# Performance work log

Hardware: AMD Instinct MI355X
Metric: run time of the kernel (lower is better)

Reference implementation:

```python
import jax, jax.numpy as jnp
import numpy as np

# Qwen3-Next gated delta-net dims
H_K, H_V, DK, DV = 16, 32, 128, 128
HID, KCONV = 2048, 4
KEY_DIM, VALUE_DIM = H_K * DK, H_V * DV      # 2048, 4096
CONV_DIM = 2 * KEY_DIM + VALUE_DIM           # 8192
GV = H_V // H_K                              # v-heads per k-head = 2
EPS = 1e-6
SEQ = 4096


def setup_inputs() -> dict:
    key = jax.random.key(0)
    ks = jax.random.split(key, 8)
    n = lambda k, sh, s: jax.random.normal(k, sh, jnp.float32) * s
    return {
        "hidden_states": n(ks[0], (SEQ, HID), 1.0),
        "W_qkvz": n(ks[1], (HID, 2 * KEY_DIM + 2 * VALUE_DIM), HID ** -0.5),
        "W_ba": n(ks[2], (HID, 2 * H_V), HID ** -0.5),
        "conv_w": n(ks[3], (CONV_DIM, KCONV), 0.5),
        "A_log": jnp.log(jax.random.uniform(ks[4], (H_V,), jnp.float32, 1.0, 16.0)),
        "dt_bias": jnp.ones((H_V,), jnp.float32),
        "norm_weight": jnp.ones((DV,), jnp.float32),
        "W_out": n(ks[5], (VALUE_DIM, HID), VALUE_DIM ** -0.5),
    }


def _l2norm(x):
    return x * jax.lax.rsqrt(jnp.sum(x * x, -1, keepdims=True) + EPS)


def reference(hidden_states, W_qkvz, W_ba, conv_w, A_log, dt_bias, norm_weight, W_out):
    L = hidden_states.shape[0]
    # 1. input projections
    qkvz = hidden_states @ W_qkvz            # (L, 12288)
    ba = hidden_states @ W_ba                # (L, 64)
    # fix_query_key_value_ordering: view per k-head group then split
    qkvz = qkvz.reshape(L, H_K, 2 * DK + 2 * GV * DV)
    q = qkvz[:, :, :DK]                                         # (L, Hk, dk)
    k = qkvz[:, :, DK:2 * DK]                                   # (L, Hk, dk)
    v = qkvz[:, :, 2 * DK:2 * DK + GV * DV].reshape(L, H_V, DV)  # (L, Hv, dv)
    z = qkvz[:, :, 2 * DK + GV * DV:].reshape(L, H_V, DV)
    ba = ba.reshape(L, H_K, 2 * GV)
    b = ba[:, :, :GV].reshape(L, H_V)
    a = ba[:, :, GV:].reshape(L, H_V)

    # 2. causal depthwise conv1d over [q|k|v] channels + silu
    mixed = jnp.concatenate([q.reshape(L, KEY_DIM), k.reshape(L, KEY_DIM),
                             v.reshape(L, VALUE_DIM)], axis=-1)  # (L, CONV_DIM)
    xp = jnp.pad(mixed, ((KCONV - 1, 0), (0, 0)))
    conv = sum(xp[i:i + L] * conv_w[:, i] for i in range(KCONV))
    mixed = jax.nn.silu(conv)

    q = mixed[:, :KEY_DIM].reshape(L, H_K, DK)
    k = mixed[:, KEY_DIM:2 * KEY_DIM].reshape(L, H_K, DK)
    v = mixed[:, 2 * KEY_DIM:].reshape(L, H_V, DV)

    # 3. fused gating: g = -exp(A_log) * softplus(a + dt_bias); beta = sigmoid(b)
    g = -jnp.exp(A_log) * jax.nn.softplus(a + dt_bias)   # (L, Hv)
    beta = jax.nn.sigmoid(b)                              # (L, Hv)

    # qk l2-norm + scale, expand k-heads to v-heads (GQA repeat)
    q = jnp.repeat(_l2norm(q), GV, axis=1) * (DK ** -0.5)  # (L, Hv, dk)
    k = jnp.repeat(_l2norm(k), GV, axis=1)

    # 4. gated delta-rule recurrence over time (state per head: dk x dv)
    def step(S, inp):
        qt, kt, vt, gt, bt = inp
        S = S * jnp.exp(gt)[:, None, None]
        kv = jnp.einsum('hkv,hk->hv', S, kt)
        delta = (vt - kv) * bt[:, None]
        S = S + kt[:, :, None] * delta[:, None, :]
        return S, jnp.einsum('hkv,hk->hv', S, qt)

    S0 = jnp.zeros((H_V, DK, DV), jnp.float32)
    _, core = jax.lax.scan(step, S0, (q, k, v, g, beta))   # (L, Hv, dv)

    # 5. gated RMSNorm (norm before gate): rmsnorm(x)*w * silu(z)
    var = jnp.mean(core * core, -1, keepdims=True)
    core = core * jax.lax.rsqrt(var + EPS) * norm_weight
    core = core * jax.nn.silu(z)

    # 6. output projection
    return core.reshape(L, VALUE_DIM) @ W_out
```

## Files before the change

kernel.cpp:

```cpp
#include <hip/hip_runtime.h>
#include <hip/hip_bf16.h>

#define SEQ 4096
#define HID 2048
#define HK_ 16
#define HV_ 32
#define KEY_DIM 2048
#define VALUE_DIM 4096
#define CONV_DIM 8192
#define NQKVZ 12288

typedef unsigned short ushort_t;
typedef short bf16x8 __attribute__((ext_vector_type(8)));
typedef float f32x4 __attribute__((ext_vector_type(4)));
typedef float f32x2 __attribute__((ext_vector_type(2)));

__device__ __forceinline__ float bf2f(ushort_t h) {
    union { unsigned int u; float f; } x; x.u = ((unsigned int)h) << 16; return x.f;
}
__device__ __forceinline__ void cvt8(uint4 v, float* f) {
    unsigned int w[4] = {v.x, v.y, v.z, v.w};
#pragma unroll
    for (int i = 0; i < 4; i++) {
        union { unsigned int u; float f; } lo, hi;
        lo.u = w[i] << 16; hi.u = w[i] & 0xffff0000u;
        f[2 * i] = lo.f; f[2 * i + 1] = hi.f;
    }
}
__device__ __forceinline__ void cvt8v(uint4 v, f32x2* f) {
    unsigned int w[4] = {v.x, v.y, v.z, v.w};
#pragma unroll
    for (int i = 0; i < 4; i++) {
        union { unsigned int u; float f; } lo, hi;
        lo.u = w[i] << 16; hi.u = w[i] & 0xffff0000u;
        f[i] = (f32x2){lo.f, hi.f};
    }
}
__device__ __forceinline__ ushort_t f2bf(float f) {
    union { float f; unsigned int u; } x; x.f = f;
    unsigned int u = x.u;
    u += 0x7fffu + ((u >> 16) & 1u);
    return (ushort_t)(u >> 16);
}

__device__ __forceinline__ void gload_lds16(const void* g, void* l) {
    __builtin_amdgcn_global_load_lds(
        (const __attribute__((address_space(1))) void*)g,
        (__attribute__((address_space(3))) void*)l, 16, 0, 0);
}
__device__ __forceinline__ void gload_lds4(const void* g, void* l) {
    __builtin_amdgcn_global_load_lds(
        (const __attribute__((address_space(1))) void*)g,
        (__attribute__((address_space(3))) void*)l, 4, 0, 0);
}

template <int CTRL>
__device__ __forceinline__ float dpp_add(float x) {
    union { float f; int i; } a, b;
    a.f = x;
    b.i = __builtin_amdgcn_update_dpp(0, a.i, CTRL, 0xF, 0xF, true);
    return a.f + b.f;
}
__device__ __forceinline__ float red16(float x) {
    x = dpp_add<0xB1>(x);
    x = dpp_add<0x4E>(x);
    x = dpp_add<0x141>(x);
    x = dpp_add<0x140>(x);
    return x;
}

__global__ void k_cvt(const float* __restrict__ src, ushort_t* __restrict__ dst)
{
    size_t i = ((size_t)blockIdx.x * 256 + threadIdx.x) * 8;
    float4 a = *(const float4*)&src[i];
    float4 b = *(const float4*)&src[i + 4];
    ushort_t u[8];
    u[0]=f2bf(a.x); u[1]=f2bf(a.y); u[2]=f2bf(a.z); u[3]=f2bf(a.w);
    u[4]=f2bf(b.x); u[5]=f2bf(b.y); u[6]=f2bf(b.z); u[7]=f2bf(b.w);
    *(uint4*)&dst[i] = *(uint4*)u;
}

__global__ __launch_bounds__(256) void k_transpose(const float* __restrict__ src,
                                                   ushort_t* __restrict__ dst,
                                                   int R, int C)
{
    __shared__ float tile[64][65];
    int c0 = blockIdx.x * 64, r0 = blockIdx.y * 64;
    int t = threadIdx.x;
    int tr = t >> 4, tc = (t & 15) * 4;
#pragma unroll
    for (int r = 0; r < 4; r++) {
        float4 v = *(const float4*)&src[(size_t)(r0 + tr + r * 16) * C + c0 + tc];
        tile[tr + r * 16][tc + 0] = v.x;
        tile[tr + r * 16][tc + 1] = v.y;
        tile[tr + r * 16][tc + 2] = v.z;
        tile[tr + r * 16][tc + 3] = v.w;
    }
    __syncthreads();
#pragma unroll
    for (int r = 0; r < 4; r++) {
        int n = c0 + tr + r * 16;
        ushort_t u[4];
#pragma unroll
        for (int i = 0; i < 4; i++) u[i] = f2bf(tile[tc + i][tr + r * 16]);
        *(uint2*)&dst[(size_t)n * R + r0 + tc] = *(uint2*)u;
    }
}

__global__ void k_ba(const float* __restrict__ A, const float* __restrict__ B,
                     const float* __restrict__ A_log, const float* __restrict__ dt_bias,
                     float* __restrict__ gbf)
{
    __shared__ float As[16][132];
    __shared__ float Bs[16][68];
    int tid = threadIdx.x;
    int m0 = blockIdx.x * 128;
    int tx = tid & 15, ty = tid >> 4;
    int arow = tid >> 2, akq = tid & 3;
    int brow = tid >> 4, bc4 = tid & 15;
    float acc[8][4];
#pragma unroll
    for (int i = 0; i < 8; i++)
#pragma unroll
        for (int j = 0; j < 4; j++) acc[i][j] = 0.f;

    for (int k0 = 0; k0 < HID; k0 += 16) {
        float4 a0 = *(const float4*)&A[(size_t)(m0 + arow) * HID + k0 + akq * 4];
        float4 a1 = *(const float4*)&A[(size_t)(m0 + arow + 64) * HID + k0 + akq * 4];
        float4 b0 = *(const float4*)&B[(size_t)(k0 + brow) * 64 + bc4 * 4];
        __syncthreads();
        As[akq * 4 + 0][arow] = a0.x; As[akq * 4 + 1][arow] = a0.y;
        As[akq * 4 + 2][arow] = a0.z; As[akq * 4 + 3][arow] = a0.w;
        As[akq * 4 + 0][arow + 64] = a1.x; As[akq * 4 + 1][arow + 64] = a1.y;
        As[akq * 4 + 2][arow + 64] = a1.z; As[akq * 4 + 3][arow + 64] = a1.w;
        *(float4*)&Bs[brow][bc4 * 4] = b0;
        __syncthreads();
#pragma unroll
        for (int kk = 0; kk < 16; kk++) {
            float xa[8], yb[4];
            *(float4*)&xa[0] = *(const float4*)&As[kk][ty * 8];
            *(float4*)&xa[4] = *(const float4*)&As[kk][ty * 8 + 4];
            *(float4*)&yb[0] = *(const float4*)&Bs[kk][tx * 4];
#pragma unroll
            for (int i = 0; i < 8; i++)
#pragma unroll
                for (int j = 0; j < 4; j++) acc[i][j] += xa[i] * yb[j];
        }
    }
#pragma unroll
    for (int i = 0; i < 8; i++) {
        int t = m0 + ty * 8 + i;
#pragma unroll
        for (int j = 0; j < 4; j++) {
            int c = tx * 4 + j;
            int hk = c >> 2, rr = c & 3;
            float val = acc[i][j];
            if (rr < 2) {
                int hv = hk * 2 + rr;
                gbf[(t * HV_ + hv) * 2 + 1] = 1.f / (1.f + expf(-val));
            } else {
                int hv = hk * 2 + (rr - 2);
                float v2 = val + dt_bias[hv];
                float sp = (v2 > 20.f) ? v2 : log1pf(expf(v2));
                float g = -expf(A_log[hv]) * sp;
                gbf[(t * HV_ + hv) * 2 + 0] = expf(g);
            }
        }
    }
}

__global__ __launch_bounds__(256) void k_gemm_qkvz(const ushort_t* __restrict__ Ab,
                                                   const ushort_t* __restrict__ Bt,
                                                   ushort_t* __restrict__ preact,
                                                   ushort_t* __restrict__ zb)
{
    __shared__ ushort_t As[128][32];
    __shared__ ushort_t Bs[128][32];
    int tid = threadIdx.x;
    int m0 = blockIdx.y * 128, n0 = blockIdx.x * 128;
    int lane = tid & 63, wave = tid >> 6;
    int wm = (wave >> 1) * 64, wn = (wave & 1) * 64;
    int quad = lane >> 4, l16 = lane & 15;

    int srow = ((wave & 1) << 6) + (lane >> 2);
    int scol = (lane & 3) << 3;
    const ushort_t* gsrc = (wave < 2)
        ? &Ab[(size_t)(m0 + srow) * HID + scol]
        : &Bt[(size_t)(n0 + srow) * HID + scol];
    ushort_t* lbase = ((wave < 2) ? &As[0][0] : &Bs[0][0]) + ((wave & 1) << 11);

    f32x4 acc[4][4];
#pragma unroll
    for (int i = 0; i < 4; i++)
#pragma unroll
        for (int j = 0; j < 4; j++) acc[i][j] = (f32x4){0.f, 0.f, 0.f, 0.f};

    for (int k0 = 0; k0 < HID; k0 += 32) {
#pragma unroll
        for (int i = 0; i < 4; i++)
            gload_lds16(gsrc + k0 + (size_t)i * 16 * HID, lbase + i * 512);
        __syncthreads();
        bf16x8 af[4], bfr[4];
#pragma unroll
        for (int i = 0; i < 4; i++) af[i]  = *(bf16x8*)&As[wm + i * 16 + l16][quad * 8];
#pragma unroll
        for (int j = 0; j < 4; j++) bfr[j] = *(bf16x8*)&Bs[wn + j * 16 + l16][quad * 8];
#pragma unroll
        for (int i = 0; i < 4; i++)
#pragma unroll
            for (int j = 0; j < 4; j++)
                acc[i][j] = __builtin_amdgcn_mfma_f32_16x16x32_bf16(af[i], bfr[j], acc[i][j], 0, 0, 0);
        __syncthreads();
    }
    int hk = n0 / 768, r = n0 % 768;
    ushort_t* dst; int ldd;
    if (r < 128)      { dst = preact + hk * 128;                    ldd = CONV_DIM; }
    else if (r < 256) { dst = preact + 2048 + hk * 128;             ldd = CONV_DIM; }
    else if (r < 512) { dst = preact + 4096 + hk * 256 + (r - 256); ldd = CONV_DIM; }
    else              { dst = zb + hk * 256 + (r - 512);            ldd = VALUE_DIM; }
#pragma unroll
    for (int i = 0; i < 4; i++)
#pragma unroll
        for (int j = 0; j < 4; j++)
#pragma unroll
            for (int rg = 0; rg < 4; rg++) {
                int m = m0 + wm + i * 16 + quad * 4 + rg;
                int n = wn + j * 16 + l16;
                dst[(size_t)m * ldd + n] = f2bf(acc[i][j][rg]);
            }
}

__global__ __launch_bounds__(256) void k_gemm_out(const ushort_t* __restrict__ Ab,
                                                  const ushort_t* __restrict__ Bt,
                                                  float* __restrict__ C)
{
    __shared__ ushort_t As[128][32];
    __shared__ ushort_t Bs[128][32];
    int tid = threadIdx.x;
    int m0 = blockIdx.y * 128, n0 = blockIdx.x * 128;
    int lane = tid & 63, wave = tid >> 6;
    int wm = (wave >> 1) * 64, wn = (wave & 1) * 64;
    int quad = lane >> 4, l16 = lane & 15;

    int srow = ((wave & 1) << 6) + (lane >> 2);
    int scol = (lane & 3) << 3;
    const ushort_t* gsrc = (wave < 2)
        ? &Ab[(size_t)(m0 + srow) * VALUE_DIM + scol]
        : &Bt[(size_t)(n0 + srow) * VALUE_DIM + scol];
    ushort_t* lbase = ((wave < 2) ? &As[0][0] : &Bs[0][0]) + ((wave & 1) << 11);

    f32x4 acc[4][4];
#pragma unroll
    for (int i = 0; i < 4; i++)
#pragma unroll
        for (int j = 0; j < 4; j++) acc[i][j] = (f32x4){0.f, 0.f, 0.f, 0.f};

    for (int k0 = 0; k0 < VALUE_DIM; k0 += 32) {
#pragma unroll
        for (int i = 0; i < 4; i++)
            gload_lds16(gsrc + k0 + (size_t)i * 16 * VALUE_DIM, lbase + i * 512);
        __syncthreads();
        bf16x8 af[4], bfr[4];
#pragma unroll
        for (int i = 0; i < 4; i++) af[i]  = *(bf16x8*)&As[wm + i * 16 + l16][quad * 8];
#pragma unroll
        for (int j = 0; j < 4; j++) bfr[j] = *(bf16x8*)&Bs[wn + j * 16 + l16][quad * 8];
#pragma unroll
        for (int i = 0; i < 4; i++)
#pragma unroll
            for (int j = 0; j < 4; j++)
                acc[i][j] = __builtin_amdgcn_mfma_f32_16x16x32_bf16(af[i], bfr[j], acc[i][j], 0, 0, 0);
        __syncthreads();
    }
#pragma unroll
    for (int i = 0; i < 4; i++)
#pragma unroll
        for (int j = 0; j < 4; j++)
#pragma unroll
            for (int rg = 0; rg < 4; rg++) {
                int m = m0 + wm + i * 16 + quad * 4 + rg;
                int n = n0 + wn + j * 16 + l16;
                C[(size_t)m * HID + n] = acc[i][j][rg];
            }
}

__global__ __launch_bounds__(256) void k_conv(const ushort_t* __restrict__ pre,
                                              const float* __restrict__ cw,
                                              ushort_t* __restrict__ qn,
                                              ushort_t* __restrict__ kn,
                                              ushort_t* __restrict__ vv)
{
    int tid = threadIdx.x;
    int c = blockIdx.x * 2048 + tid * 8;
    int t0 = blockIdx.y * 4;
    float w[8][4];
#pragma unroll
    for (int j = 0; j < 8; j++)
        *(float4*)w[j] = *(const float4*)&cw[(size_t)(c + j) * 4];
    float p[7][8];
#pragma unroll
    for (int i = 0; i < 7; i++) {
        int tt = t0 + i - 3;
        if (tt >= 0) {
            uint4 v = *(const uint4*)&pre[(size_t)tt * CONV_DIM + c];
            cvt8(v, p[i]);
        } else {
#pragma unroll
            for (int j = 0; j < 8; j++) p[i][j] = 0.f;
        }
    }
    float x[4][8];
#pragma unroll
    for (int u = 0; u < 4; u++)
#pragma unroll
        for (int j = 0; j < 8; j++) {
            float a = p[u][j] * w[j][0] + p[u + 1][j] * w[j][1]
                    + p[u + 2][j] * w[j][2] + p[u + 3][j] * w[j][3];
            x[u][j] = a / (1.f + expf(-a));
        }
    if (blockIdx.x < 2) {
        bool isq = (blockIdx.x == 0);
        float headscale = isq ? 0.08838834764831845f : 1.f;
        ushort_t* dst = isq ? qn : kn;
        int cc = isq ? c : (c - KEY_DIM);
#pragma unroll
        for (int u = 0; u < 4; u++) {
            float ss = 0.f;
#pragma unroll
            for (int j = 0; j < 8; j++) ss += x[u][j] * x[u][j];
            ss = red16(ss);
            float mul = headscale / sqrtf(ss + 1e-6f);
            ushort_t o[8];
#pragma unroll
            for (int j = 0; j < 8; j++) o[j] = f2bf(x[u][j] * mul);
            *(uint4*)&dst[(size_t)(t0 + u) * KEY_DIM + cc] = *(uint4*)o;
        }
    } else {
        int cc = c - 2 * KEY_DIM;
#pragma unroll
        for (int u = 0; u < 4; u++) {
            ushort_t o[8];
#pragma unroll
            for (int j = 0; j < 8; j++) o[j] = f2bf(x[u][j]);
            *(uint4*)&vv[(size_t)(t0 + u) * VALUE_DIM + cc] = *(uint4*)o;
        }
    }
}

__global__ __launch_bounds__(256) void k_recur(const ushort_t* __restrict__ qn,
                                               const ushort_t* __restrict__ kn,
                                               const ushort_t* __restrict__ vv,
                                               const float2* __restrict__ gb,
                                               float* __restrict__ core)
{
    __shared__ ushort_t Ks[2][32][128];
    __shared__ ushort_t Qs[2][32][128];
    __shared__ ushort_t Vs[2][32][16];
    __shared__ float    Gs[2][32][2];
    int tid = threadIdx.x;
    int h = blockIdx.y;
    int hk = h >> 1;
    int kc = tid & 15;
    int cl = tid >> 4;
    bool lead = (kc == 0);
    int lane = tid & 63, wave = tid >> 6;

    const ushort_t* kh = kn + hk * 128;
    const ushort_t* qh = qn + hk * 128;
    const ushort_t* vh = vv + h * 128 + blockIdx.x * 16;
    const float*    gh = (const float*)(gb + h);
    float* outp = core + h * 128 + blockIdx.x * 16 + cl;

    auto stage = [&](int bi, int t0) {
        if (wave < 2) {
            int rb = wave * 16;
#pragma unroll
            for (int c = 0; c < 4; c++) {
                int r = rb + c * 4 + (lane >> 4);
                gload_lds16(kh + (size_t)(t0 + r) * KEY_DIM + (lane & 15) * 8,
                            &Ks[bi][rb + c * 4][0]);
            }
#pragma unroll
            for (int c = 0; c < 2; c++) {
                int r = rb + c * 8 + (lane >> 3);
                gload_lds4(vh + (size_t)(t0 + r) * VALUE_DIM + (lane & 7) * 2,
                           &Vs[bi][rb + c * 8][0]);
            }
        } else {
            int rb = (wave - 2) * 16;
#pragma unroll
            for (int c = 0; c < 4; c++) {
                int r = rb + c * 4 + (lane >> 4);
                gload_lds16(qh + (size_t)(t0 + r) * KEY_DIM + (lane & 15) * 8,
                            &Qs[bi][rb + c * 4][0]);
            }
            if (wave == 2) {
                int r = lane >> 1;
                gload_lds4(gh + (size_t)(t0 + r) * (HV_ * 2) + (lane & 1),
                           &Gs[bi][0][0]);
            }
        }
    };

    f32x2 S_[4];
#pragma unroll
    for (int j = 0; j < 4; j++) S_[j] = (f32x2){0.f, 0.f};

    stage(0, 0);
    __syncthreads();

    for (int tc = 0; tc < SEQ / 32; tc++) {
        int bi = tc & 1;
        if (tc + 1 < SEQ / 32) stage(bi ^ 1, (tc + 1) * 32);
        int t0 = tc * 32;
#pragma unroll 8
        for (int s = 0; s < 32; s++) {
            uint4 kvr = *(const uint4*)&Ks[bi][s][kc * 8];
            uint4 qvr = *(const uint4*)&Qs[bi][s][kc * 8];
            f32x2 k2[4], q2[4];
            cvt8v(kvr, k2);
            cvt8v(qvr, q2);
            float v_ = bf2f(Vs[bi][s][cl]);
            float e = Gs[bi][s][0], b = Gs[bi][s][1];
            f32x2 acc = S_[0] * k2[0];
            acc += S_[1] * k2[1];
            acc += S_[2] * k2[2];
            acc += S_[3] * k2[3];
            float d1 = red16(acc.x + acc.y);
            float dl = (v_ - e * d1) * b;
            f32x2 e2 = (f32x2){e, e}, dl2 = (f32x2){dl, dl};
            f32x2 oacc = (f32x2){0.f, 0.f};
#pragma unroll
            for (int j = 0; j < 4; j++) {
                S_[j] = S_[j] * e2 + k2[j] * dl2;
                oacc += S_[j] * q2[j];
            }
            float o = red16(oacc.x + oacc.y);
            if (lead) outp[(size_t)(t0 + s) * VALUE_DIM] = o;
        }
        __syncthreads();
    }
}

__global__ void k_gate(const float* __restrict__ core, const ushort_t* __restrict__ z,
                       const float* __restrict__ nw, ushort_t* __restrict__ corebf)
{
    __shared__ float red[2];
    int hv = blockIdx.x, t = blockIdx.y, d = threadIdx.x;
    size_t idx = (size_t)t * VALUE_DIM + hv * 128 + d;
    float cval = core[idx];
    float ss = cval * cval;
    for (int m = 32; m >= 1; m >>= 1) ss += __shfl_xor(ss, m, 64);
    int wv = d >> 6, ln = d & 63;
    if (ln == 0) red[wv] = ss;
    __syncthreads();
    float var = (red[0] + red[1]) * (1.f / 128.f);
    float zv = bf2f(z[idx]);
    float out = cval * (1.f / sqrtf(var + 1e-6f)) * nw[d] * (zv / (1.f + expf(-zv)));
    corebf[idx] = f2bf(out);
}

extern "C" void kernel_launch(void* const* d_in, const int* in_sizes, int n_in,
                              void* d_out, int out_size, void* d_ws, size_t ws_size,
                              hipStream_t stream)
{
    const float* hs    = (const float*)d_in[0];
    const float* Wqkvz = (const float*)d_in[1];
    const float* Wba   = (const float*)d_in[2];
    const float* convw = (const float*)d_in[3];
    const float* Alog  = (const float*)d_in[4];
    const float* dtb   = (const float*)d_in[5];
    const float* nw    = (const float*)d_in[6];
    const float* Wout  = (const float*)d_in[7];
    float* out = (float*)d_out;

    char* w = (char*)d_ws;
    ushort_t* preact = (ushort_t*)w;
    float*    coreb  = (float*)w;
    w += (size_t)SEQ * CONV_DIM * 2;
    ushort_t* zb = (ushort_t*)w;  w += (size_t)SEQ * VALUE_DIM * 2;
    float* gbf   = (float*)w;     w += (size_t)SEQ * HV_ * 8;
    ushort_t* qnb = (ushort_t*)w; w += (size_t)SEQ * KEY_DIM * 2;
    ushort_t* knb = (ushort_t*)w; w += (size_t)SEQ * KEY_DIM * 2;
    ushort_t* vvb = (ushort_t*)w; w += (size_t)SEQ * VALUE_DIM * 2;
    size_t needed = (size_t)(w - (char*)d_ws);
    if (ws_size < needed) return;

    ushort_t* wqT    = qnb;
    ushort_t* hsb    = qnb + (size_t)24 * 1024 * 1024;
    ushort_t* woutT  = vvb;
    ushort_t* corebf = qnb;

    hipLaunchKernelGGL(k_ba, dim3(32), dim3(256), 0, stream, hs, Wba, Alog, dtb, gbf);
    hipLaunchKernelGGL(k_cvt, dim3(4096), dim3(256), 0, stream, hs, hsb);
    hipLaunchKernelGGL(k_transpose, dim3(192, 32), dim3(256), 0, stream, Wqkvz, wqT, HID, NQKVZ);
    hipLaunchKernelGGL(k_gemm_qkvz, dim3(96, 32), dim3(256), 0, stream, hsb, wqT, preact, zb);
    hipLaunchKernelGGL(k_conv, dim3(4, 1024), dim3(256), 0, stream, preact, convw, qnb, knb, vvb);
    hipLaunchKernelGGL(k_recur, dim3(8, 32), dim3(256), 0, stream, qnb, knb, vvb,
                       (const float2*)gbf, coreb);
    hipLaunchKernelGGL(k_transpose, dim3(32, 64), dim3(256), 0, stream, Wout, woutT, VALUE_DIM, HID);
    hipLaunchKernelGGL(k_gate, dim3(32, 4096), dim3(128), 0, stream, coreb, zb, nw, corebf);
    hipLaunchKernelGGL(k_gemm_out, dim3(16, 32), dim3(256), 0, stream, corebf, woutT, out);
}
```

Before: 1.561 ms.

## Process both GQA v-heads per block in recurrence to share K/Q loads

The recurrence kernel now handles the two value heads that share one key head inside a single block: each thread keeps two state slices and reuses the same K and Q vectors from shared memory for both. Blocks shrink to 128 threads covering 8 value columns per head, on a 16x16 grid, so the total block count stays at 256. This halves redundant K/Q global and LDS traffic per unit of work and adds independent instruction streams per thread to hide reduction latency. The cost is fewer threads per block, more registers, and longer serial per-step work per thread.

```diff
diff --git a/kernel.cpp b/kernel.cpp
--- a/kernel.cpp
+++ b/kernel.cpp
@@ -347,7 +347,7 @@
     }
 }
 
-__global__ __launch_bounds__(256) void k_recur(const ushort_t* __restrict__ qn,
+__global__ __launch_bounds__(128) void k_recur(const ushort_t* __restrict__ qn,
                                                const ushort_t* __restrict__ kn,
                                                const ushort_t* __restrict__ vv,
                                                const float2* __restrict__ gb,
@@ -355,56 +355,57 @@
 {
     __shared__ ushort_t Ks[2][32][128];
     __shared__ ushort_t Qs[2][32][128];
-    __shared__ ushort_t Vs[2][32][16];
-    __shared__ float    Gs[2][32][2];
+    __shared__ ushort_t Vs[2][32][2][8];
+    __shared__ float    Gs[2][32][2][2];
     int tid = threadIdx.x;
-    int h = blockIdx.y;
-    int hk = h >> 1;
+    int hp = blockIdx.y;
     int kc = tid & 15;
     int cl = tid >> 4;
     bool lead = (kc == 0);
     int lane = tid & 63, wave = tid >> 6;
 
-    const ushort_t* kh = kn + hk * 128;
-    const ushort_t* qh = qn + hk * 128;
-    const ushort_t* vh = vv + h * 128 + blockIdx.x * 16;
-    const float*    gh = (const float*)(gb + h);
-    float* outp = core + h * 128 + blockIdx.x * 16 + cl;
+    const ushort_t* kh = kn + hp * 128;
+    const ushort_t* qh = qn + hp * 128;
+    const ushort_t* vh = vv + (size_t)(2 * hp) * 128 + blockIdx.x * 8;
+    const float*    gh = (const float*)gb;
+    float* outp0 = core + (size_t)(2 * hp) * 128 + blockIdx.x * 8 + cl;
+    float* outp1 = outp0 + 128;
 
     auto stage = [&](int bi, int t0) {
-        if (wave < 2) {
-            int rb = wave * 16;
+        if (wave == 0) {
+#pragma unroll
+            for (int c = 0; c < 8; c++) {
+                int r = c * 4 + (lane >> 4);
+                gload_lds16(kh + (size_t)(t0 + r) * KEY_DIM + (lane & 15) * 8,
+                            &Ks[bi][c * 4][0]);
+            }
 #pragma unroll
             for (int c = 0; c < 4; c++) {
-                int r = rb + c * 4 + (lane >> 4);
-                gload_lds16(kh + (size_t)(t0 + r) * KEY_DIM + (lane & 15) * 8,
-                            &Ks[bi][rb + c * 4][0]);
+                int u = c * 64 + lane;
+                int t = u >> 3, hh = (u >> 2) & 1, cp = u & 3;
+                gload_lds4(vh + (size_t)(t0 + t) * VALUE_DIM + hh * 128 + cp * 2,
+                           &Vs[bi][c * 8][0][0]);
+            }
+        } else {
+#pragma unroll
+            for (int c = 0; c < 8; c++) {
+                int r = c * 4 + (lane >> 4);
+                gload_lds16(qh + (size_t)(t0 + r) * KEY_DIM + (lane & 15) * 8,
+                            &Qs[bi][c * 4][0]);
             }
 #pragma unroll
             for (int c = 0; c < 2; c++) {
-                int r = rb + c * 8 + (lane >> 3);
-                gload_lds4(vh + (size_t)(t0 + r) * VALUE_DIM + (lane & 7) * 2,
-                           &Vs[bi][rb + c * 8][0]);
-            }
-        } else {
-            int rb = (wave - 2) * 16;
-#pragma unroll
-            for (int c = 0; c < 4; c++) {
-                int r = rb + c * 4 + (lane >> 4);
-                gload_lds16(qh + (size_t)(t0 + r) * KEY_DIM + (lane & 15) * 8,
-                            &Qs[bi][rb + c * 4][0]);
-            }
-            if (wave == 2) {
-                int r = lane >> 1;
-                gload_lds4(gh + (size_t)(t0 + r) * (HV_ * 2) + (lane & 1),
-                           &Gs[bi][0][0]);
+                int u = c * 64 + lane;
+                int t = u >> 2, hh = (u >> 1) & 1, ww = u & 1;
+                gload_lds4(gh + ((size_t)(t0 + t) * HV_ + 2 * hp + hh) * 2 + ww,
+                           &Gs[bi][c * 16][0][0]);
             }
         }
     };
 
-    f32x2 S_[4];
-#pragma unroll
-    for (int j = 0; j < 4; j++) S_[j] = (f32x2){0.f, 0.f};
+    f32x2 S0_[4], S1_[4];
+#pragma unroll
+    for (int j = 0; j < 4; j++) { S0_[j] = (f32x2){0.f, 0.f}; S1_[j] = (f32x2){0.f, 0.f}; }
 
     stage(0, 0);
     __syncthreads();
@@ -420,23 +421,37 @@
             f32x2 k2[4], q2[4];
             cvt8v(kvr, k2);
             cvt8v(qvr, q2);
-            float v_ = bf2f(Vs[bi][s][cl]);
-            float e = Gs[bi][s][0], b = Gs[bi][s][1];
-            f32x2 acc = S_[0] * k2[0];
-            acc += S_[1] * k2[1];
-            acc += S_[2] * k2[2];
-            acc += S_[3] * k2[3];
-            float d1 = red16(acc.x + acc.y);
-            float dl = (v_ - e * d1) * b;
-            f32x2 e2 = (f32x2){e, e}, dl2 = (f32x2){dl, dl};
-            f32x2 oacc = (f32x2){0.f, 0.f};
+            float v0 = bf2f(Vs[bi][s][0][cl]);
+            float v1 = bf2f(Vs[bi][s][1][cl]);
+            float e0 = Gs[bi][s][0][0], b0 = Gs[bi][s][0][1];
+            float e1 = Gs[bi][s][1][0], b1 = Gs[bi][s][1][1];
+            f32x2 aA0 = S0_[0] * k2[0];
+            f32x2 aA1 = S1_[0] * k2[0];
+#pragma unroll
+            for (int j = 1; j < 4; j++) {
+                aA0 += S0_[j] * k2[j];
+                aA1 += S1_[j] * k2[j];
+            }
+            float rA0 = red16(aA0.x + aA0.y);
+            float rA1 = red16(aA1.x + aA1.y);
+            float dl0 = (v0 - e0 * rA0) * b0;
+            float dl1 = (v1 - e1 * rA1) * b1;
+            f32x2 e20 = (f32x2){e0, e0}, dl20 = (f32x2){dl0, dl0};
+            f32x2 e21 = (f32x2){e1, e1}, dl21 = (f32x2){dl1, dl1};
+            f32x2 oa0 = (f32x2){0.f, 0.f}, oa1 = (f32x2){0.f, 0.f};
 #pragma unroll
             for (int j = 0; j < 4; j++) {
-                S_[j] = S_[j] * e2 + k2[j] * dl2;
-                oacc += S_[j] * q2[j];
-            }
-            float o = red16(oacc.x + oacc.y);
-            if (lead) outp[(size_t)(t0 + s) * VALUE_DIM] = o;
+                S0_[j] = S0_[j] * e20 + k2[j] * dl20;
+                oa0 += S0_[j] * q2[j];
+                S1_[j] = S1_[j] * e21 + k2[j] * dl21;
+                oa1 += S1_[j] * q2[j];
+            }
+            float o0 = red16(oa0.x + oa0.y);
+            float o1 = red16(oa1.x + oa1.y);
+            if (lead) {
+                outp0[(size_t)(t0 + s) * VALUE_DIM] = o0;
+                outp1[(size_t)(t0 + s) * VALUE_DIM] = o1;
+            }
         }
         __syncthreads();
     }
@@ -496,7 +511,7 @@
     hipLaunchKernelGGL(k_transpose, dim3(192, 32), dim3(256), 0, stream, Wqkvz, wqT, HID, NQKVZ);
     hipLaunchKernelGGL(k_gemm_qkvz, dim3(96, 32), dim3(256), 0, stream, hsb, wqT, preact, zb);
     hipLaunchKernelGGL(k_conv, dim3(4, 1024), dim3(256), 0, stream, preact, convw, qnb, knb, vvb);
-    hipLaunchKernelGGL(k_recur, dim3(8, 32), dim3(256), 0, stream, qnb, knb, vvb,
+    hipLaunchKernelGGL(k_recur, dim3(16, 16), dim3(128), 0, stream, qnb, knb, vvb,
                        (const float2*)gbf, coreb);
     hipLaunchKernelGGL(k_transpose, dim3(32, 64), dim3(256), 0, stream, Wout, woutT, VALUE_DIM, HID);
     hipLaunchKernelGGL(k_gate, dim3(32, 4096), dim3(128), 0, stream, coreb, zb, nw, corebf);
```

New measurement: 1.846 ms. 1.18x slower.

## Split recurrence state across 32 lanes per column, doubling blocks

Applied to the files above, without the earlier changes.

The delta-rule recurrence kernel now gives each state column 32 lanes of 4 dk elements each, where before it used 16 lanes of 8. Partial sums are combined with a permlane32 swap after the DPP reduction, and each block covers 8 value columns instead of 16, so the grid doubles to 16x32 blocks. This shortens the serial per-step dependency chain and raises the number of active blocks on this latency-bound sequential scan. The cost is an extra cross-lane exchange per reduction and twice as many redundant K/Q loads into LDS across blocks.

```diff
diff --git a/kernel.cpp b/kernel.cpp
--- a/kernel.cpp
+++ b/kernel.cpp
@@ -14,6 +14,7 @@
 typedef short bf16x8 __attribute__((ext_vector_type(8)));
 typedef float f32x4 __attribute__((ext_vector_type(4)));
 typedef float f32x2 __attribute__((ext_vector_type(2)));
+typedef unsigned int u32x2 __attribute__((ext_vector_type(2)));
 
 __device__ __forceinline__ float bf2f(ushort_t h) {
     union { unsigned int u; float f; } x; x.u = ((unsigned int)h) << 16; return x.f;
@@ -27,10 +28,10 @@
         f[2 * i] = lo.f; f[2 * i + 1] = hi.f;
     }
 }
-__device__ __forceinline__ void cvt8v(uint4 v, f32x2* f) {
-    unsigned int w[4] = {v.x, v.y, v.z, v.w};
-#pragma unroll
-    for (int i = 0; i < 4; i++) {
+__device__ __forceinline__ void cvt4v2(uint2 v, f32x2* f) {
+    unsigned int w[2] = {v.x, v.y};
+#pragma unroll
+    for (int i = 0; i < 2; i++) {
         union { unsigned int u; float f; } lo, hi;
         lo.u = w[i] << 16; hi.u = w[i] & 0xffff0000u;
         f[i] = (f32x2){lo.f, hi.f};
@@ -67,6 +68,13 @@
     x = dpp_add<0x141>(x);
     x = dpp_add<0x140>(x);
     return x;
+}
+__device__ __forceinline__ float cross32_add(float x) {
+    union { float f; unsigned int u; } a; a.f = x;
+    u32x2 r = __builtin_amdgcn_permlane32_swap(a.u, a.u, false, false);
+    union { unsigned int u; float f; } p, q;
+    p.u = r[0]; q.u = r[1];
+    return p.f + q.f;
 }
 
 __global__ void k_cvt(const float* __restrict__ src, ushort_t* __restrict__ dst)
@@ -355,21 +363,22 @@
 {
     __shared__ ushort_t Ks[2][32][128];
     __shared__ ushort_t Qs[2][32][128];
-    __shared__ ushort_t Vs[2][32][16];
+    __shared__ ushort_t Vs[2][32][8];
     __shared__ float    Gs[2][32][2];
     int tid = threadIdx.x;
     int h = blockIdx.y;
     int hk = h >> 1;
-    int kc = tid & 15;
-    int cl = tid >> 4;
+    int lane = tid & 63, wave = tid >> 6;
+    int g = (lane >> 4) & 1;
+    int kc = (lane & 15) | ((lane >> 5) << 4);
+    int colw = wave * 2 + g;
     bool lead = (kc == 0);
-    int lane = tid & 63, wave = tid >> 6;
 
     const ushort_t* kh = kn + hk * 128;
     const ushort_t* qh = qn + hk * 128;
-    const ushort_t* vh = vv + h * 128 + blockIdx.x * 16;
+    const ushort_t* vh = vv + (size_t)h * 128 + blockIdx.x * 8;
     const float*    gh = (const float*)(gb + h);
-    float* outp = core + h * 128 + blockIdx.x * 16 + cl;
+    float* outp = core + (size_t)h * 128 + blockIdx.x * 8 + colw;
 
     auto stage = [&](int bi, int t0) {
         if (wave < 2) {
@@ -380,11 +389,10 @@
                 gload_lds16(kh + (size_t)(t0 + r) * KEY_DIM + (lane & 15) * 8,
                             &Ks[bi][rb + c * 4][0]);
             }
-#pragma unroll
-            for (int c = 0; c < 2; c++) {
-                int r = rb + c * 8 + (lane >> 3);
-                gload_lds4(vh + (size_t)(t0 + r) * VALUE_DIM + (lane & 7) * 2,
-                           &Vs[bi][rb + c * 8][0]);
+            {
+                int r = wave * 16 + (lane >> 2);
+                gload_lds4(vh + (size_t)(t0 + r) * VALUE_DIM + (lane & 3) * 2,
+                           &Vs[bi][wave * 16][0]);
             }
         } else {
             int rb = (wave - 2) * 16;
@@ -402,9 +410,9 @@
         }
     };
 
-    f32x2 S_[4];
-#pragma unroll
-    for (int j = 0; j < 4; j++) S_[j] = (f32x2){0.f, 0.f};
+    f32x2 S_[2];
+    S_[0] = (f32x2){0.f, 0.f};
+    S_[1] = (f32x2){0.f, 0.f};
 
     stage(0, 0);
     __syncthreads();
@@ -415,27 +423,25 @@
         int t0 = tc * 32;
 #pragma unroll 8
         for (int s = 0; s < 32; s++) {
-            uint4 kvr = *(const uint4*)&Ks[bi][s][kc * 8];
-            uint4 qvr = *(const uint4*)&Qs[bi][s][kc * 8];
-            f32x2 k2[4], q2[4];
-            cvt8v(kvr, k2);
-            cvt8v(qvr, q2);
-            float v_ = bf2f(Vs[bi][s][cl]);
+            uint2 kvr = *(const uint2*)&Ks[bi][s][kc * 4];
+            uint2 qvr = *(const uint2*)&Qs[bi][s][kc * 4];
+            f32x2 k2[2], q2[2];
+            cvt4v2(kvr, k2);
+            cvt4v2(qvr, q2);
+            float v_ = bf2f(Vs[bi][s][colw]);
             float e = Gs[bi][s][0], b = Gs[bi][s][1];
-            f32x2 acc = S_[0] * k2[0];
-            acc += S_[1] * k2[1];
-            acc += S_[2] * k2[2];
-            acc += S_[3] * k2[3];
-            float d1 = red16(acc.x + acc.y);
-            float dl = (v_ - e * d1) * b;
+            f32x2 aA = S_[0] * k2[0];
+            aA += S_[1] * k2[1];
+            float rA = cross32_add(red16(aA.x + aA.y));
+            float dl = (v_ - e * rA) * b;
             f32x2 e2 = (f32x2){e, e}, dl2 = (f32x2){dl, dl};
             f32x2 oacc = (f32x2){0.f, 0.f};
 #pragma unroll
-            for (int j = 0; j < 4; j++) {
+            for (int j = 0; j < 2; j++) {
                 S_[j] = S_[j] * e2 + k2[j] * dl2;
                 oacc += S_[j] * q2[j];
             }
-            float o = red16(oacc.x + oacc.y);
+            float o = cross32_add(red16(oacc.x + oacc.y));
             if (lead) outp[(size_t)(t0 + s) * VALUE_DIM] = o;
         }
         __syncthreads();
@@ -496,7 +502,7 @@
     hipLaunchKernelGGL(k_transpose, dim3(192, 32), dim3(256), 0, stream, Wqkvz, wqT, HID, NQKVZ);
     hipLaunchKernelGGL(k_gemm_qkvz, dim3(96, 32), dim3(256), 0, stream, hsb, wqT, preact, zb);
     hipLaunchKernelGGL(k_conv, dim3(4, 1024), dim3(256), 0, stream, preact, convw, qnb, knb, vvb);
-    hipLaunchKernelGGL(k_recur, dim3(8, 32), dim3(256), 0, stream, qnb, knb, vvb,
+    hipLaunchKernelGGL(k_recur, dim3(16, 32), dim3(256), 0, stream, qnb, knb, vvb,
                        (const float2*)gbf, coreb);
     hipLaunchKernelGGL(k_transpose, dim3(32, 64), dim3(256), 0, stream, Wout, woutT, VALUE_DIM, HID);
     hipLaunchKernelGGL(k_gate, dim3(32, 4096), dim3(128), 0, stream, coreb, zb, nw, corebf);
```

After: 1.691 ms. 1.08x slower.
